# Optimization experiments

Measured on AMD Instinct MI355X. Metric: run time of the kernel, lower is better.

The kernel has to match this reference:

```python
import jax, jax.numpy as jnp
import numpy as np

N = 4096      # particles
E = 262144    # interacting pairs (~64 neighbors each)
H = 128       # MLP hidden width
FD = 6        # force/velocity DOF (force + torque)
FEAT = 7      # rel(3) + dist + r_sq + r_quad + min_dist
IN_DIM = FEAT + 2 * FD  # 19


def setup_inputs() -> dict:
    key = jax.random.key(0)
    ks = jax.random.split(key, 10)
    rel_vecs = jax.random.normal(ks[0], (N, N, 3), jnp.float32)
    target_indices = jax.random.randint(ks[1], (E,), 0, N, dtype=jnp.int64)
    source_indices = jax.random.randint(ks[2], (E,), 0, N, dtype=jnp.int64)
    force = jax.random.normal(ks[3], (N, FD), jnp.float32)
    viscosity = jnp.ones((1,), jnp.float32)
    s1 = 1.0 / np.sqrt(IN_DIM)
    s2 = 1.0 / np.sqrt(H)
    W1 = jax.random.normal(ks[4], (IN_DIM, H), jnp.float32) * s1
    b1 = jnp.zeros((H,), jnp.float32)
    W2 = jax.random.normal(ks[5], (H, H), jnp.float32) * s2
    b2 = jnp.zeros((H,), jnp.float32)
    W3 = jax.random.normal(ks[6], (H, FD), jnp.float32) * s2
    b3 = jnp.zeros((FD,), jnp.float32)
    median = jnp.float32(2.5)
    contact_distance = jnp.float32(2.0)
    return {
        'rel_vecs': rel_vecs, 'target_indices': target_indices,
        'source_indices': source_indices, 'force': force,
        'viscosity': viscosity, 'median': median,
        'contact_distance': contact_distance,
        'W1': W1, 'b1': b1, 'W2': W2, 'b2': b2, 'W3': W3, 'b3': b3,
    }


def _predict_velocity(features, f_t, f_s, mu, W1, b1, W2, b2, W3, b3):
    # MLP over concatenated pair features + both forces; Stokes flow is
    # linear in force/viscosity, so scale output by 1/mu.
    x = jnp.concatenate([features, f_t, f_s], axis=-1)  # [E, 19]
    h = jax.nn.relu(x @ W1 + b1)
    h = jax.nn.relu(h @ W2 + b2)
    return (h @ W3 + b3) / mu  # [E, FD]


def reference(rel_vecs, target_indices, source_indices, force, viscosity,
              median, contact_distance, W1, b1, W2, b2, W3, b3):
    # Gather pairwise relative vectors: [E, 3]
    rel_selected = rel_vecs[target_indices, source_indices]
    dist = jnp.maximum(
        jnp.linalg.norm(rel_selected, axis=-1, keepdims=True), 1e-8)  # [E,1]
    r_shift = dist - median
    r_sq = r_shift * r_shift
    r_quad = r_sq * r_sq
    min_dist = dist - contact_distance
    features = jnp.concatenate(
        [rel_selected, dist, r_sq, r_quad, min_dist], axis=-1)  # [E, 7]
    force_target = force[target_indices]  # [E, FD]
    force_source = force[source_indices]  # [E, FD]
    mu = jnp.asarray(viscosity, dtype=force.dtype).reshape(())
    vel = _predict_velocity(features, force_target, force_source, mu,
                            W1, b1, W2, b2, W3, b3)  # [E, FD]
    # Scatter-add per-target contributions
    contribution = jnp.zeros_like(force).at[target_indices].add(vel)
    return contribution
```

## Files before the change

### kernel.cpp

```cpp
#include <hip/hip_runtime.h>

#define NPART 4096
#define E_TOT 262144
#define HID   128
#define FDOF  6
#define BM    64
#define NIT   (E_TOT / BM)
#define GRID  1024
#define XPAD  40
#define HPAD  136

typedef __bf16 bf16x8 __attribute__((ext_vector_type(8)));
typedef float  f32x4  __attribute__((ext_vector_type(4)));

__global__ void pairvel_zero_kernel(float* __restrict__ out, int n) {
    const int i = blockIdx.x * blockDim.x + threadIdx.x;
    if (i < n) out[i] = 0.0f;
}

__global__ __launch_bounds__(256) void pairvel_mfma_kernel(
    const float* __restrict__ rel,
    const int*   __restrict__ tgt,
    const int*   __restrict__ src,
    const float* __restrict__ force,
    const float* __restrict__ visc,
    const float* __restrict__ medianp,
    const float* __restrict__ contactp,
    const float* __restrict__ W1,
    const float* __restrict__ b1,
    const float* __restrict__ W2,
    const float* __restrict__ b2,
    const float* __restrict__ W3,
    const float* __restrict__ b3,
    float* __restrict__ out)
{
    const int tid = threadIdx.x;
    const int w   = tid >> 6;
    const int l   = tid & 63;
    const int l15 = l & 15;
    const int lhi = l >> 4;

    bf16x8 w1f[2], w2f[4][2], w3f[4];
    #pragma unroll
    for (int nb = 0; nb < 2; ++nb) {
        const int n = (2 * w + nb) * 16 + l15;
        #pragma unroll
        for (int r = 0; r < 8; ++r) {
            const int k = lhi * 8 + r;
            w1f[nb][r] = (k < 19) ? (__bf16)W1[k * HID + n] : (__bf16)0.0f;
        }
    }
    #pragma unroll
    for (int kt = 0; kt < 4; ++kt)
        #pragma unroll
        for (int nb = 0; nb < 2; ++nb) {
            const int n = (2 * w + nb) * 16 + l15;
            #pragma unroll
            for (int r = 0; r < 8; ++r)
                w2f[kt][nb][r] = (__bf16)W2[(kt * 32 + lhi * 8 + r) * HID + n];
        }
    #pragma unroll
    for (int kt = 0; kt < 4; ++kt)
        #pragma unroll
        for (int r = 0; r < 8; ++r) {
            const int k = kt * 32 + lhi * 8 + r;
            w3f[kt][r] = (l15 < FDOF) ? (__bf16)W3[k * FDOF + l15] : (__bf16)0.0f;
        }

    const float b1v0 = b1[(2 * w) * 16 + l15];
    const float b1v1 = b1[(2 * w + 1) * 16 + l15];
    const float b2v0 = b2[(2 * w) * 16 + l15];
    const float b2v1 = b2[(2 * w + 1) * 16 + l15];
    const float b3v  = (l15 < FDOF) ? b3[l15] : 0.0f;
    const float inv_mu  = 1.0f / visc[0];
    const float median  = medianp[0];
    const float contact = contactp[0];

    __shared__ __align__(16) __bf16 Xs[BM][XPAD];
    __shared__ __align__(16) __bf16 H1s[BM][HPAD];
    __shared__ __align__(16) __bf16 H2s[BM][HPAD];
    __shared__ int tgts[BM];

    for (int t = tid; t < BM * 13; t += 256) {
        const int e = t / 13, c = 19 + t % 13;
        Xs[e][c] = (__bf16)0.0f;
    }

    for (int it = blockIdx.x; it < NIT; it += GRID) {
        const int e0 = it * BM;
        __syncthreads();

        if (tid < BM) {
            const int e = tid, eg = e0 + e;
            const int tg = tgt[eg], sg = src[eg];
            tgts[e] = tg;
            const float* rp = rel + ((size_t)tg * NPART + sg) * 3;
            const float x0 = rp[0], x1 = rp[1], x2 = rp[2];
            const float dist =
                fmaxf(sqrtf(x0 * x0 + x1 * x1 + x2 * x2), 1e-8f);
            const float rs = (dist - median) * (dist - median);
            Xs[e][0] = (__bf16)x0;
            Xs[e][1] = (__bf16)x1;
            Xs[e][2] = (__bf16)x2;
            Xs[e][3] = (__bf16)dist;
            Xs[e][4] = (__bf16)rs;
            Xs[e][5] = (__bf16)(rs * rs);
            Xs[e][6] = (__bf16)(dist - contact);
        } else if (tid < 2 * BM) {
            const int e = tid - BM;
            const int tg = tgt[e0 + e];
            #pragma unroll
            for (int d = 0; d < FDOF; ++d)
                Xs[e][7 + d] = (__bf16)force[tg * FDOF + d];
        } else if (tid < 3 * BM) {
            const int e = tid - 2 * BM;
            const int sg = src[e0 + e];
            #pragma unroll
            for (int d = 0; d < FDOF; ++d)
                Xs[e][13 + d] = (__bf16)force[sg * FDOF + d];
        }
        __syncthreads();

        #pragma unroll
        for (int m = 0; m < 4; ++m) {
            const bf16x8 a =
                *reinterpret_cast<const bf16x8*>(&Xs[m * 16 + l15][lhi * 8]);
            #pragma unroll
            for (int nb = 0; nb < 2; ++nb) {
                const float bv = nb ? b1v1 : b1v0;
                f32x4 acc = { bv, bv, bv, bv };
                acc = __builtin_amdgcn_mfma_f32_16x16x32_bf16(
                          a, w1f[nb], acc, 0, 0, 0);
                #pragma unroll
                for (int r = 0; r < 4; ++r)
                    H1s[m * 16 + lhi * 4 + r][(2 * w + nb) * 16 + l15] =
                        (__bf16)fmaxf(acc[r], 0.0f);
            }
        }
        __syncthreads();

        #pragma unroll
        for (int m = 0; m < 4; ++m) {
            f32x4 acc0 = { b2v0, b2v0, b2v0, b2v0 };
            f32x4 acc1 = { b2v1, b2v1, b2v1, b2v1 };
            #pragma unroll
            for (int kt = 0; kt < 4; ++kt) {
                const bf16x8 a = *reinterpret_cast<const bf16x8*>(
                    &H1s[m * 16 + l15][kt * 32 + lhi * 8]);
                acc0 = __builtin_amdgcn_mfma_f32_16x16x32_bf16(
                           a, w2f[kt][0], acc0, 0, 0, 0);
                acc1 = __builtin_amdgcn_mfma_f32_16x16x32_bf16(
                           a, w2f[kt][1], acc1, 0, 0, 0);
            }
            #pragma unroll
            for (int r = 0; r < 4; ++r) {
                H2s[m * 16 + lhi * 4 + r][(2 * w) * 16 + l15] =
                    (__bf16)fmaxf(acc0[r], 0.0f);
                H2s[m * 16 + lhi * 4 + r][(2 * w + 1) * 16 + l15] =
                    (__bf16)fmaxf(acc1[r], 0.0f);
            }
        }
        __syncthreads();

        f32x4 acc3 = { 0.0f, 0.0f, 0.0f, 0.0f };
        #pragma unroll
        for (int kt = 0; kt < 4; ++kt) {
            const bf16x8 a = *reinterpret_cast<const bf16x8*>(
                &H2s[w * 16 + l15][kt * 32 + lhi * 8]);
            acc3 = __builtin_amdgcn_mfma_f32_16x16x32_bf16(
                       a, w3f[kt], acc3, 0, 0, 0);
        }
        if (l15 < FDOF) {
            #pragma unroll
            for (int r = 0; r < 4; ++r) {
                const int e = w * 16 + lhi * 4 + r;
                atomicAdd(&out[(size_t)tgts[e] * FDOF + l15],
                          (acc3[r] + b3v) * inv_mu);
            }
        }
    }
}

extern "C" void kernel_launch(void* const* d_in, const int* in_sizes, int n_in,
                              void* d_out, int out_size, void* d_ws, size_t ws_size,
                              hipStream_t stream) {
    const float* rel   = (const float*)d_in[0];
    const int*   tgt   = (const int*)d_in[1];
    const int*   src   = (const int*)d_in[2];
    const float* force = (const float*)d_in[3];
    const float* visc  = (const float*)d_in[4];
    const float* med   = (const float*)d_in[5];
    const float* con   = (const float*)d_in[6];
    const float* W1    = (const float*)d_in[7];
    const float* b1    = (const float*)d_in[8];
    const float* W2    = (const float*)d_in[9];
    const float* b2    = (const float*)d_in[10];
    const float* W3    = (const float*)d_in[11];
    const float* b3    = (const float*)d_in[12];
    float* out = (float*)d_out;

    pairvel_zero_kernel<<<(out_size + 255) / 256, 256, 0, stream>>>(out, out_size);
    pairvel_mfma_kernel<<<GRID, 256, 0, stream>>>(
        rel, tgt, src, force, visc, med, con, W1, b1, W2, b2, W3, b3, out);
}
```

Baseline: 47.63 us.

## Double-buffer gathered pair features to overlap loads with MLP compute

The input feature tile becomes double-buffered. The next tile's scattered gathers (rel vectors, indices, forces) are issued into registers during layer 1, then written to the alternate shared buffer during layer 2. This hides gather latency behind the MFMA work. Force loads become float2 vector loads, the grid shrinks to 768 blocks, and XPAD grows to 48. The cost is more registers and shared memory, which could lower occupancy.

```diff
diff --git a/kernel.cpp b/kernel.cpp
--- a/kernel.cpp
+++ b/kernel.cpp
@@ -6,8 +6,8 @@
 #define FDOF  6
 #define BM    64
 #define NIT   (E_TOT / BM)
-#define GRID  1024
-#define XPAD  40
+#define GRID  768
+#define XPAD  48
 #define HPAD  136
 
 typedef __bf16 bf16x8 __attribute__((ext_vector_type(8)));
@@ -76,55 +76,88 @@
     const float median  = medianp[0];
     const float contact = contactp[0];
 
-    __shared__ __align__(16) __bf16 Xs[BM][XPAD];
+    __shared__ __align__(16) __bf16 Xs[2][BM][XPAD];
     __shared__ __align__(16) __bf16 H1s[BM][HPAD];
     __shared__ __align__(16) __bf16 H2s[BM][HPAD];
-    __shared__ int tgts[BM];
-
-    for (int t = tid; t < BM * 13; t += 256) {
-        const int e = t / 13, c = 19 + t % 13;
-        Xs[e][c] = (__bf16)0.0f;
+    __shared__ int tgts[2][BM];
+
+    for (int t = tid; t < 2 * BM * 13; t += 256) {
+        const int b = t / (BM * 13), rem = t % (BM * 13);
+        Xs[b][rem / 13][19 + rem % 13] = (__bf16)0.0f;
     }
 
-    for (int it = blockIdx.x; it < NIT; it += GRID) {
-        const int e0 = it * BM;
-        __syncthreads();
-
+    int   p_i0 = 0;
+    float p_v0 = 0.f, p_v1 = 0.f, p_v2 = 0.f;
+    float p_f3 = 0.f, p_f4 = 0.f, p_f5 = 0.f;
+
+    auto gather_load = [&](int e0n) {
         if (tid < BM) {
-            const int e = tid, eg = e0 + e;
-            const int tg = tgt[eg], sg = src[eg];
-            tgts[e] = tg;
-            const float* rp = rel + ((size_t)tg * NPART + sg) * 3;
-            const float x0 = rp[0], x1 = rp[1], x2 = rp[2];
-            const float dist =
-                fmaxf(sqrtf(x0 * x0 + x1 * x1 + x2 * x2), 1e-8f);
+            const int eg = e0n + tid;
+            p_i0 = tgt[eg];
+            const int sg = src[eg];
+            const float* rp = rel + ((size_t)p_i0 * NPART + sg) * 3;
+            p_v0 = rp[0]; p_v1 = rp[1]; p_v2 = rp[2];
+        } else if (tid < 2 * BM) {
+            const int eg = e0n + (tid - BM);
+            const float2* f2 =
+                reinterpret_cast<const float2*>(force + (size_t)tgt[eg] * FDOF);
+            const float2 u0 = f2[0], u1 = f2[1], u2 = f2[2];
+            p_v0 = u0.x; p_v1 = u0.y; p_v2 = u1.x;
+            p_f3 = u1.y; p_f4 = u2.x; p_f5 = u2.y;
+        } else if (tid < 3 * BM) {
+            const int eg = e0n + (tid - 2 * BM);
+            const float2* f2 =
+                reinterpret_cast<const float2*>(force + (size_t)src[eg] * FDOF);
+            const float2 u0 = f2[0], u1 = f2[1], u2 = f2[2];
+            p_v0 = u0.x; p_v1 = u0.y; p_v2 = u1.x;
+            p_f3 = u1.y; p_f4 = u2.x; p_f5 = u2.y;
+        }
+    };
+
+    auto write_x = [&](int b) {
+        if (tid < BM) {
+            const int e = tid;
+            tgts[b][e] = p_i0;
+            const float dist = fmaxf(
+                sqrtf(p_v0 * p_v0 + p_v1 * p_v1 + p_v2 * p_v2), 1e-8f);
             const float rs = (dist - median) * (dist - median);
-            Xs[e][0] = (__bf16)x0;
-            Xs[e][1] = (__bf16)x1;
-            Xs[e][2] = (__bf16)x2;
-            Xs[e][3] = (__bf16)dist;
-            Xs[e][4] = (__bf16)rs;
-            Xs[e][5] = (__bf16)(rs * rs);
-            Xs[e][6] = (__bf16)(dist - contact);
+            Xs[b][e][0] = (__bf16)p_v0;
+            Xs[b][e][1] = (__bf16)p_v1;
+            Xs[b][e][2] = (__bf16)p_v2;
+            Xs[b][e][3] = (__bf16)dist;
+            Xs[b][e][4] = (__bf16)rs;
+            Xs[b][e][5] = (__bf16)(rs * rs);
+            Xs[b][e][6] = (__bf16)(dist - contact);
         } else if (tid < 2 * BM) {
             const int e = tid - BM;
-            const int tg = tgt[e0 + e];
-            #pragma unroll
-            for (int d = 0; d < FDOF; ++d)
-                Xs[e][7 + d] = (__bf16)force[tg * FDOF + d];
+            Xs[b][e][7]  = (__bf16)p_v0;
+            Xs[b][e][8]  = (__bf16)p_v1;
+            Xs[b][e][9]  = (__bf16)p_v2;
+            Xs[b][e][10] = (__bf16)p_f3;
+            Xs[b][e][11] = (__bf16)p_f4;
+            Xs[b][e][12] = (__bf16)p_f5;
         } else if (tid < 3 * BM) {
             const int e = tid - 2 * BM;
-            const int sg = src[e0 + e];
-            #pragma unroll
-            for (int d = 0; d < FDOF; ++d)
-                Xs[e][13 + d] = (__bf16)force[sg * FDOF + d];
-        }
+            Xs[b][e][13] = (__bf16)p_v0;
+            Xs[b][e][14] = (__bf16)p_v1;
+            Xs[b][e][15] = (__bf16)p_v2;
+            Xs[b][e][16] = (__bf16)p_f3;
+            Xs[b][e][17] = (__bf16)p_f4;
+            Xs[b][e][18] = (__bf16)p_f5;
+        }
+    };
+
+    gather_load(blockIdx.x * BM);
+    write_x(0);
+    int buf = 0;
+
+    for (int it = blockIdx.x; it < NIT; it += GRID) {
         __syncthreads();
 
         #pragma unroll
         for (int m = 0; m < 4; ++m) {
-            const bf16x8 a =
-                *reinterpret_cast<const bf16x8*>(&Xs[m * 16 + l15][lhi * 8]);
+            const bf16x8 a = *reinterpret_cast<const bf16x8*>(
+                &Xs[buf][m * 16 + l15][lhi * 8]);
             #pragma unroll
             for (int nb = 0; nb < 2; ++nb) {
                 const float bv = nb ? b1v1 : b1v0;
@@ -137,6 +170,10 @@
                         (__bf16)fmaxf(acc[r], 0.0f);
             }
         }
+
+        const bool havenext = (it + GRID) < NIT;
+        if (havenext) gather_load((it + GRID) * BM);
+
         __syncthreads();
 
         #pragma unroll
@@ -160,6 +197,9 @@
                     (__bf16)fmaxf(acc1[r], 0.0f);
             }
         }
+
+        if (havenext) write_x(buf ^ 1);
+
         __syncthreads();
 
         f32x4 acc3 = { 0.0f, 0.0f, 0.0f, 0.0f };
@@ -174,10 +214,11 @@
             #pragma unroll
             for (int r = 0; r < 4; ++r) {
                 const int e = w * 16 + lhi * 4 + r;
-                atomicAdd(&out[(size_t)tgts[e] * FDOF + l15],
+                atomicAdd(&out[(size_t)tgts[buf][e] * FDOF + l15],
                           (acc3[r] + b3v) * inv_mu);
             }
         }
+        buf ^= 1;
     }
 }
 
```

Result: slower. 54.49 us (+14.4%).

## Keep MLP activations in registers per wave via transposed MFMA and lane shuffles

Applied to the files above, without the earlier changes.

Restructures the kernel so each wave independently processes 32-edge tiles, computing transposed products (weights as the A operand) so layer outputs stay in registers and are re-packed into the next layer's operand with cross-half lane shuffles instead of round-tripping through shared memory with block-wide barriers. W2 is staged once into LDS in a swizzled fragment layout, b1 is folded into W1 through a constant-one input column, and the gather for the next tile is issued early to overlap its memory latency with compute. This removes per-tile __syncthreads and LDS activation traffic, at the cost of higher register pressure and LDS reads of W2 on every tile.

```diff
diff --git a/kernel.cpp b/kernel.cpp
--- a/kernel.cpp
+++ b/kernel.cpp
@@ -4,18 +4,24 @@
 #define E_TOT 262144
 #define HID   128
 #define FDOF  6
-#define BM    64
-#define NIT   (E_TOT / BM)
-#define GRID  1024
-#define XPAD  40
-#define HPAD  136
+#define WE    32
+#define NWT   (E_TOT / WE)
+#define GRID  512
+#define NW    (GRID * 4)
 
 typedef __bf16 bf16x8 __attribute__((ext_vector_type(8)));
 typedef float  f32x4  __attribute__((ext_vector_type(4)));
+typedef unsigned int uint32x4 __attribute__((ext_vector_type(4)));
 
 __global__ void pairvel_zero_kernel(float* __restrict__ out, int n) {
     const int i = blockIdx.x * blockDim.x + threadIdx.x;
     if (i < n) out[i] = 0.0f;
+}
+
+static __device__ __forceinline__ unsigned int pack2(float a, float b) {
+    const unsigned short ua = __builtin_bit_cast(unsigned short, (__bf16)a);
+    const unsigned short ub = __builtin_bit_cast(unsigned short, (__bf16)b);
+    return (unsigned int)ua | ((unsigned int)ub << 16);
 }
 
 __global__ __launch_bounds__(256) void pairvel_mfma_kernel(
@@ -39,143 +45,217 @@
     const int l   = tid & 63;
     const int l15 = l & 15;
     const int lhi = l >> 4;
-
-    bf16x8 w1f[2], w2f[4][2], w3f[4];
-    #pragma unroll
-    for (int nb = 0; nb < 2; ++nb) {
-        const int n = (2 * w + nb) * 16 + l15;
+    const bool islow = (l < 32);
+
+    __shared__ __align__(16) __bf16 W2L[4][8][64][8];
+
+    #pragma unroll
+    for (int i = 0; i < 8; ++i) {
+        const int entry = i * 256 + tid;
+        const int kt = entry >> 9;
+        const int nb = (entry >> 6) & 7;
+        const int ln = entry & 63;
+        const int sl15 = ln & 15, slhi = ln >> 4;
+        const int base1 = (slhi & 1) * 4 + (slhi & 2) * 12;
+        const int base2 = 8 + (slhi & 1) * 4 + (slhi & 2) * 4;
+        bf16x8 v;
         #pragma unroll
         for (int r = 0; r < 8; ++r) {
-            const int k = lhi * 8 + r;
-            w1f[nb][r] = (k < 19) ? (__bf16)W1[k * HID + n] : (__bf16)0.0f;
-        }
+            const int row = kt * 32 + ((r < 4) ? (base1 + r) : (base2 + r - 4));
+            v[r] = (__bf16)W2[row * HID + nb * 16 + sl15];
+        }
+        *reinterpret_cast<bf16x8*>(&W2L[kt][nb][ln][0]) = v;
     }
+
+    bf16x8 w1A[8];
+    #pragma unroll
+    for (int nb = 0; nb < 8; ++nb)
+        #pragma unroll
+        for (int r = 0; r < 8; ++r) {
+            const int c = lhi * 8 + r;
+            float v = 0.0f;
+            if (c < 19) { const int ko = (c < 12) ? c + 7 : c - 12;
+                          v = W1[ko * HID + nb * 16 + l15]; }
+            else if (c == 31) v = b1[nb * 16 + l15];
+            w1A[nb][r] = (__bf16)v;
+        }
+
+    const int base1 = (lhi & 1) * 4 + (lhi & 2) * 12;
+    const int base2 = 8 + (lhi & 1) * 4 + (lhi & 2) * 4;
+    bf16x8 w3A[4];
     #pragma unroll
     for (int kt = 0; kt < 4; ++kt)
         #pragma unroll
-        for (int nb = 0; nb < 2; ++nb) {
-            const int n = (2 * w + nb) * 16 + l15;
-            #pragma unroll
-            for (int r = 0; r < 8; ++r)
-                w2f[kt][nb][r] = (__bf16)W2[(kt * 32 + lhi * 8 + r) * HID + n];
-        }
-    #pragma unroll
-    for (int kt = 0; kt < 4; ++kt)
-        #pragma unroll
         for (int r = 0; r < 8; ++r) {
-            const int k = kt * 32 + lhi * 8 + r;
-            w3f[kt][r] = (l15 < FDOF) ? (__bf16)W3[k * FDOF + l15] : (__bf16)0.0f;
-        }
-
-    const float b1v0 = b1[(2 * w) * 16 + l15];
-    const float b1v1 = b1[(2 * w + 1) * 16 + l15];
-    const float b2v0 = b2[(2 * w) * 16 + l15];
-    const float b2v1 = b2[(2 * w + 1) * 16 + l15];
-    const float b3v  = (l15 < FDOF) ? b3[l15] : 0.0f;
+            const int row = kt * 32 + ((r < 4) ? (base1 + r) : (base2 + r - 4));
+            w3A[kt][r] = (l15 < FDOF) ? (__bf16)W3[row * FDOF + l15]
+                                      : (__bf16)0.0f;
+        }
+
+    f32x4 b2i[8];
+    #pragma unroll
+    for (int nb = 0; nb < 8; ++nb)
+        b2i[nb] = *reinterpret_cast<const f32x4*>(&b2[nb * 16 + lhi * 4]);
+    float b3i[4];
+    #pragma unroll
+    for (int r = 0; r < 4; ++r) {
+        const int d = lhi * 4 + r;
+        b3i[r] = (d < FDOF) ? b3[d] : 0.0f;
+    }
     const float inv_mu  = 1.0f / visc[0];
     const float median  = medianp[0];
     const float contact = contactp[0];
 
-    __shared__ __align__(16) __bf16 Xs[BM][XPAD];
-    __shared__ __align__(16) __bf16 H1s[BM][HPAD];
-    __shared__ __align__(16) __bf16 H2s[BM][HPAD];
-    __shared__ int tgts[BM];
-
-    for (int t = tid; t < BM * 13; t += 256) {
-        const int e = t / 13, c = 19 + t % 13;
-        Xs[e][c] = (__bf16)0.0f;
-    }
-
-    for (int it = blockIdx.x; it < NIT; it += GRID) {
-        const int e0 = it * BM;
-        __syncthreads();
-
-        if (tid < BM) {
-            const int e = tid, eg = e0 + e;
-            const int tg = tgt[eg], sg = src[eg];
-            tgts[e] = tg;
-            const float* rp = rel + ((size_t)tg * NPART + sg) * 3;
-            const float x0 = rp[0], x1 = rp[1], x2 = rp[2];
-            const float dist =
-                fmaxf(sqrtf(x0 * x0 + x1 * x1 + x2 * x2), 1e-8f);
-            const float rs = (dist - median) * (dist - median);
-            Xs[e][0] = (__bf16)x0;
-            Xs[e][1] = (__bf16)x1;
-            Xs[e][2] = (__bf16)x2;
-            Xs[e][3] = (__bf16)dist;
-            Xs[e][4] = (__bf16)rs;
-            Xs[e][5] = (__bf16)(rs * rs);
-            Xs[e][6] = (__bf16)(dist - contact);
-        } else if (tid < 2 * BM) {
-            const int e = tid - BM;
-            const int tg = tgt[e0 + e];
-            #pragma unroll
-            for (int d = 0; d < FDOF; ++d)
-                Xs[e][7 + d] = (__bf16)force[tg * FDOF + d];
-        } else if (tid < 3 * BM) {
-            const int e = tid - 2 * BM;
-            const int sg = src[e0 + e];
-            #pragma unroll
-            for (int d = 0; d < FDOF; ++d)
-                Xs[e][13 + d] = (__bf16)force[sg * FDOF + d];
-        }
-        __syncthreads();
-
-        #pragma unroll
-        for (int m = 0; m < 4; ++m) {
-            const bf16x8 a =
-                *reinterpret_cast<const bf16x8*>(&Xs[m * 16 + l15][lhi * 8]);
-            #pragma unroll
-            for (int nb = 0; nb < 2; ++nb) {
-                const float bv = nb ? b1v1 : b1v0;
-                f32x4 acc = { bv, bv, bv, bv };
-                acc = __builtin_amdgcn_mfma_f32_16x16x32_bf16(
-                          a, w1f[nb], acc, 0, 0, 0);
+    __syncthreads();
+
+    int   pft[2];
+    float pf[2][8];
+
+    auto gather_issue = [&](int tile) {
+        #pragma unroll
+        for (int g = 0; g < 2; ++g) {
+            if (lhi < 3) {
+                const int eg = tile * WE + g * 16 + l15;
+                const int tg = tgt[eg];
+                const int sg = src[eg];
+                pft[g] = tg;
+                if (lhi == 0) {
+                    const float2* ft = (const float2*)(force + tg * FDOF);
+                    const float2* fs = (const float2*)(force + sg * FDOF);
+                    const float2 a = ft[0], b = ft[1], c = ft[2], d = fs[0];
+                    pf[g][0] = a.x; pf[g][1] = a.y; pf[g][2] = b.x;
+                    pf[g][3] = b.y; pf[g][4] = c.x; pf[g][5] = c.y;
+                    pf[g][6] = d.x; pf[g][7] = d.y;
+                } else if (lhi == 1) {
+                    const float2* fs = (const float2*)(force + sg * FDOF);
+                    const float2 a = fs[1], b = fs[2];
+                    const float* rp = rel + ((size_t)tg * NPART + sg) * 3;
+                    pf[g][0] = a.x;  pf[g][1] = a.y;
+                    pf[g][2] = b.x;  pf[g][3] = b.y;
+                    pf[g][4] = rp[0]; pf[g][5] = rp[1]; pf[g][6] = rp[2];
+                } else {
+                    const float* rp = rel + ((size_t)tg * NPART + sg) * 3;
+                    pf[g][0] = rp[0]; pf[g][1] = rp[1]; pf[g][2] = rp[2];
+                }
+            }
+        }
+    };
+
+    auto build_xb = [&](int g) -> bf16x8 {
+        float x0=0,x1=0,x2=0,x3=0,x4=0,x5=0,x6=0,x7=0;
+        if (lhi == 0) {
+            x0=pf[g][0]; x1=pf[g][1]; x2=pf[g][2]; x3=pf[g][3];
+            x4=pf[g][4]; x5=pf[g][5]; x6=pf[g][6]; x7=pf[g][7];
+        } else if (lhi == 1) {
+            x0=pf[g][0]; x1=pf[g][1]; x2=pf[g][2]; x3=pf[g][3];
+            const float r0=pf[g][4], r1=pf[g][5], r2=pf[g][6];
+            const float dist = fmaxf(sqrtf(r0*r0+r1*r1+r2*r2), 1e-8f);
+            x4=r0; x5=r1; x6=r2; x7=dist;
+        } else if (lhi == 2) {
+            const float r0=pf[g][0], r1=pf[g][1], r2=pf[g][2];
+            const float dist = fmaxf(sqrtf(r0*r0+r1*r1+r2*r2), 1e-8f);
+            const float rsh = dist - median;
+            const float rs  = rsh * rsh;
+            x0=rs; x1=rs*rs; x2=dist-contact;
+        } else {
+            x7 = 1.0f;
+        }
+        return (bf16x8){ (__bf16)x0,(__bf16)x1,(__bf16)x2,(__bf16)x3,
+                         (__bf16)x4,(__bf16)x5,(__bf16)x6,(__bf16)x7 };
+    };
+
+    auto exchange = [&](unsigned pe_lo, unsigned pe_hi,
+                        unsigned po_lo, unsigned po_hi) -> bf16x8 {
+        const unsigned w0 = islow ? pe_lo : po_lo;
+        const unsigned w1 = islow ? pe_hi : po_hi;
+        const unsigned s2 = islow ? po_lo : pe_lo;
+        const unsigned s3 = islow ? po_hi : pe_hi;
+        const unsigned w2 = (unsigned)__shfl_xor((int)s2, 32, 64);
+        const unsigned w3 = (unsigned)__shfl_xor((int)s3, 32, 64);
+        return __builtin_bit_cast(bf16x8, (uint32x4){w0, w1, w2, w3});
+    };
+
+    const int gw = blockIdx.x * 4 + w;
+    gather_issue(gw);
+
+    for (int tile = gw; tile < NWT; tile += NW) {
+        const bf16x8 xb0 = build_xb(0);
+        const bf16x8 xb1 = build_xb(1);
+        const int tga0 = pft[0], tga1 = pft[1];
+        if (tile + NW < NWT) gather_issue(tile + NW);
+
+        bf16x8 h1b[2][4];
+        #pragma unroll
+        for (int q = 0; q < 4; ++q) {
+            unsigned pe_lo[2], pe_hi[2], po_lo[2], po_hi[2];
+            #pragma unroll
+            for (int par = 0; par < 2; ++par) {
+                const int nb = 2 * q + par;
                 #pragma unroll
-                for (int r = 0; r < 4; ++r)
-                    H1s[m * 16 + lhi * 4 + r][(2 * w + nb) * 16 + l15] =
-                        (__bf16)fmaxf(acc[r], 0.0f);
-            }
-        }
-        __syncthreads();
-
-        #pragma unroll
-        for (int m = 0; m < 4; ++m) {
-            f32x4 acc0 = { b2v0, b2v0, b2v0, b2v0 };
-            f32x4 acc1 = { b2v1, b2v1, b2v1, b2v1 };
-            #pragma unroll
-            for (int kt = 0; kt < 4; ++kt) {
-                const bf16x8 a = *reinterpret_cast<const bf16x8*>(
-                    &H1s[m * 16 + l15][kt * 32 + lhi * 8]);
-                acc0 = __builtin_amdgcn_mfma_f32_16x16x32_bf16(
-                           a, w2f[kt][0], acc0, 0, 0, 0);
-                acc1 = __builtin_amdgcn_mfma_f32_16x16x32_bf16(
-                           a, w2f[kt][1], acc1, 0, 0, 0);
-            }
-            #pragma unroll
-            for (int r = 0; r < 4; ++r) {
-                H2s[m * 16 + lhi * 4 + r][(2 * w) * 16 + l15] =
-                    (__bf16)fmaxf(acc0[r], 0.0f);
-                H2s[m * 16 + lhi * 4 + r][(2 * w + 1) * 16 + l15] =
-                    (__bf16)fmaxf(acc1[r], 0.0f);
-            }
-        }
-        __syncthreads();
-
-        f32x4 acc3 = { 0.0f, 0.0f, 0.0f, 0.0f };
+                for (int g = 0; g < 2; ++g) {
+                    f32x4 acc = {0.f, 0.f, 0.f, 0.f};
+                    acc = __builtin_amdgcn_mfma_f32_16x16x32_bf16(
+                              w1A[nb], g ? xb1 : xb0, acc, 0, 0, 0);
+                    const unsigned lo = pack2(fmaxf(acc[0],0.f), fmaxf(acc[1],0.f));
+                    const unsigned hi = pack2(fmaxf(acc[2],0.f), fmaxf(acc[3],0.f));
+                    if (par == 0) { pe_lo[g] = lo; pe_hi[g] = hi; }
+                    else          { po_lo[g] = lo; po_hi[g] = hi; }
+                }
+            }
+            #pragma unroll
+            for (int g = 0; g < 2; ++g)
+                h1b[g][q] = exchange(pe_lo[g], pe_hi[g], po_lo[g], po_hi[g]);
+        }
+
+        bf16x8 h2b[2][4];
+        #pragma unroll
+        for (int q = 0; q < 4; ++q) {
+            unsigned pe_lo[2], pe_hi[2], po_lo[2], po_hi[2];
+            #pragma unroll
+            for (int par = 0; par < 2; ++par) {
+                const int nb = 2 * q + par;
+                f32x4 acc0 = b2i[nb];
+                f32x4 acc1 = b2i[nb];
+                #pragma unroll
+                for (int kt = 0; kt < 4; ++kt) {
+                    const bf16x8 wa = *reinterpret_cast<const bf16x8*>(
+                        &W2L[kt][nb][l][0]);
+                    acc0 = __builtin_amdgcn_mfma_f32_16x16x32_bf16(
+                               wa, h1b[0][kt], acc0, 0, 0, 0);
+                    acc1 = __builtin_amdgcn_mfma_f32_16x16x32_bf16(
+                               wa, h1b[1][kt], acc1, 0, 0, 0);
+                }
+                const unsigned lo0 = pack2(fmaxf(acc0[0],0.f), fmaxf(acc0[1],0.f));
+                const unsigned hi0 = pack2(fmaxf(acc0[2],0.f), fmaxf(acc0[3],0.f));
+                const unsigned lo1 = pack2(fmaxf(acc1[0],0.f), fmaxf(acc1[1],0.f));
+                const unsigned hi1 = pack2(fmaxf(acc1[2],0.f), fmaxf(acc1[3],0.f));
+                if (par == 0) { pe_lo[0]=lo0; pe_hi[0]=hi0; pe_lo[1]=lo1; pe_hi[1]=hi1; }
+                else          { po_lo[0]=lo0; po_hi[0]=hi0; po_lo[1]=lo1; po_hi[1]=hi1; }
+            }
+            #pragma unroll
+            for (int g = 0; g < 2; ++g)
+                h2b[g][q] = exchange(pe_lo[g], pe_hi[g], po_lo[g], po_hi[g]);
+        }
+
+        f32x4 acc30 = {0.f,0.f,0.f,0.f}, acc31 = {0.f,0.f,0.f,0.f};
         #pragma unroll
         for (int kt = 0; kt < 4; ++kt) {
-            const bf16x8 a = *reinterpret_cast<const bf16x8*>(
-                &H2s[w * 16 + l15][kt * 32 + lhi * 8]);
-            acc3 = __builtin_amdgcn_mfma_f32_16x16x32_bf16(
-                       a, w3f[kt], acc3, 0, 0, 0);
-        }
-        if (l15 < FDOF) {
-            #pragma unroll
-            for (int r = 0; r < 4; ++r) {
-                const int e = w * 16 + lhi * 4 + r;
-                atomicAdd(&out[(size_t)tgts[e] * FDOF + l15],
-                          (acc3[r] + b3v) * inv_mu);
+            acc30 = __builtin_amdgcn_mfma_f32_16x16x32_bf16(
+                        w3A[kt], h2b[0][kt], acc30, 0, 0, 0);
+            acc31 = __builtin_amdgcn_mfma_f32_16x16x32_bf16(
+                        w3A[kt], h2b[1][kt], acc31, 0, 0, 0);
+        }
+
+        if (lhi < 2) {
+            #pragma unroll
+            for (int j = 0; j < 4; ++j) {
+                const int d = lhi * 4 + j;
+                if (d < FDOF) {
+                    atomicAdd(&out[(size_t)tga0 * FDOF + d],
+                              (acc30[j] + b3i[j]) * inv_mu);
+                    atomicAdd(&out[(size_t)tga1 * FDOF + d],
+                              (acc31[j] + b3i[j]) * inv_mu);
+                }
             }
         }
     }
```

Result: slower. 100.5 us (+111.0%).
